# Performance work log

Hardware: AMD Instinct MI355X
Metric: run time of the kernel (lower is better)

Reference implementation:

```python
import jax, jax.numpy as jnp
import numpy as np

N = 118; DM = 768; DP = 128; DR = 128; DH = 256; DN = 256; DPHI = 192; DE = 256; NOUT = 2
T = 2048; NFEAT = 64
NEG = 0.01  # LeakyReLU default slope


def leaky(x):
    return jax.nn.leaky_relu(x, NEG)


def lstm(x, Wih, Whh, bih, bhh, last_only=False):
    # x: [B,T,F]; PyTorch gate order i,f,g,o
    B, Tt, _ = x.shape
    H = Whh.shape[1]
    xg = x @ Wih.T + (bih + bhh)  # [B,T,4H] precomputed input gates
    def step(carry, xt):
        h, c = carry
        g = xt + h @ Whh.T
        i, f, gg, o = jnp.split(g, 4, axis=-1)
        c = jax.nn.sigmoid(f) * c + jax.nn.sigmoid(i) * jnp.tanh(gg)
        h = jax.nn.sigmoid(o) * jnp.tanh(c)
        return (h, c), (None if last_only else h)
    init = (jnp.zeros((B, H), x.dtype), jnp.zeros((B, H), x.dtype))
    (h, c), hs = jax.lax.scan(step, init, jnp.swapaxes(xg, 0, 1))
    return h if last_only else jnp.swapaxes(hs, 0, 1)


def setup_inputs() -> dict:
    key = jax.random.key(0)
    ks = iter(jax.random.split(key, 40))
    def rn(shape, scale=0.05):
        return jax.random.normal(next(ks), shape, jnp.float32) * scale
    inp = {
        'x': jax.random.normal(next(ks), (N, T, NFEAT), jnp.float32),
        'x_message': jax.random.normal(next(ks), (N, DM), jnp.float32),
        'pseudo_message': rn((DM,), 1.0),
        'Wih0': rn((4 * DP, NFEAT)), 'Whh0': rn((4 * DP, DP)), 'bih0': rn((4 * DP,)), 'bhh0': rn((4 * DP,)),
        'Wih1': rn((4 * DP, DP)), 'Whh1': rn((4 * DP, DP)), 'bih1': rn((4 * DP,)), 'bhh1': rn((4 * DP,)),
        'Wum': rn((DM + 1, DR)), 'Wvm': rn((DM + 1, DR)),
        'Wup': rn((DP + 1, DR)), 'Wvp': rn((DP + 1, DR)),
        'Wpe': rn((2, 3 * DR)), 'bpe': rn((2,)),
        'Whyb': rn((DH, 3 * DR)), 'bhyb': rn((DH,)),
        'Wact': rn((DN, DH + 2)), 'bact': rn((DN,)),
        'Winact': rn((DN, DH)), 'binact': rn((DN,)),
        'Wphin': rn((2 * DN, DPHI)), 'aphi': rn((DPHI, 1)),
        'Won': rn((2 * DN, DN)), 'Weo': rn((3 * DN, DE)),
        'Wi': rn((N, DN + 2 * DE, NOUT)), 'bi': rn((N, NOUT)),
    }
    return inp


def reference(x, x_message, pseudo_message, Wih0, Whh0, bih0, bhh0, Wih1, Whh1, bih1, bhh1,
              Wum, Wvm, Wup, Wvp, Wpe, bpe, Whyb, bhyb, Wact, bact, Winact, binact,
              Wphin, aphi, Won, Weo, Wi, bi):
    h1 = lstm(x, Wih0, Whh0, bih0, bhh0)
    p = leaky(lstm(h1, Wih1, Whh1, bih1, bhh1, last_only=True))  # [N,DP]
    status = (jnp.sum(x_message, axis=-1) == 0).astype(x.dtype)  # [N]
    m = jnp.where(status[:, None] == 1, pseudo_message[None, :], x_message)
    st = status[:, None]  # [N,1]
    mc = jnp.concatenate([m, st], axis=1)
    pc = jnp.concatenate([p, st], axis=1)
    u_m = leaky(mc @ Wum); v_m = leaky(mc @ Wvm)
    u_p = leaky(pc @ Wup); v_p = leaky(pc @ Wvp)
    h_pmt = jax.nn.softmax(jnp.concatenate([u_m, u_m * v_p, v_p], 1) @ Wpe.T + bpe, axis=1)
    h_hyb = leaky(jnp.concatenate([u_p, u_p + v_m, v_m], 1) @ Whyb.T + bhyb)
    n_act = (jnp.concatenate([h_hyb, h_pmt], 1) @ Wact.T + bact) * (1 - st)
    n_in = (h_hyb @ Winact.T + binact) * st
    n = leaky(n_act + n_in)  # [N,DN]
    # pair[i,j] = concat(n[j], n[i]) matching torch repeat pattern
    pair = jnp.concatenate([jnp.broadcast_to(n[None, :, :], (N, N, DN)),
                            jnp.broadcast_to(n[:, None, :], (N, N, DN))], axis=-1)
    phi = (leaky(pair @ Wphin) @ aphi)[..., 0]  # [N,N]
    V1 = status == 0; V0 = status == 1
    def gsm(ph, mask):  # softmax over selected rows, per column
        logits = jnp.where(mask[:, None], ph, -1e30)
        return jnp.where(mask[:, None], jax.nn.softmax(logits, axis=0), ph)
    alpha = gsm(gsm(phi, V1), V0)
    e = jnp.concatenate([leaky(pair @ Won), pair], axis=-1) @ Weo  # [N,N,DE]
    hm1 = leaky(jnp.einsum('ij,ijd->id', (1 - st) * alpha, e))
    hm0 = leaky(jnp.einsum('ij,ijd->id', st * alpha, e))
    output = jnp.concatenate([n, hm0, hm1], axis=-1)  # [N, DN+2*DE]
    y_hat = jax.nn.softmax(jnp.einsum('nd,ndo->no', output, Wi) + bi, axis=1)
    l_ort = jnp.sqrt(jnp.sum((Wum @ Wvm.T) ** 2)) + jnp.sqrt(jnp.sum((Wup @ Wvp.T) ** 2))
    # vectorized pairwise cosine-sim * sign polarity over V1 nodes
    a = h_pmt[:, 1] - h_pmt[:, 0]
    w = jnp.where(V1, jnp.sign(a), 0.0)
    nn_ = n / jnp.maximum(jnp.linalg.norm(n, axis=1, keepdims=True), 1e-8)
    l_pol = jnp.sum((nn_ @ nn_.T) * (w[:, None] * w[None, :]))
    return y_hat, h_pmt, l_ort, l_pol
```

## Files before the change

kernel.cpp:

```cpp
#include <hip/hip_runtime.h>
#include <hip/hip_bf16.h>
#include <math.h>

#define NN 118
#define TT 2048
#define NF 64
#define DP 128
#define DN 256

typedef float v2f __attribute__((ext_vector_type(2)));

__device__ __forceinline__ float leaky(float x) { return x > 0.f ? x : 0.01f * x; }

__device__ __forceinline__ float waveRedSum(float v) {
#pragma unroll
    for (int off = 32; off > 0; off >>= 1) v += __shfl_down(v, off, 64);
    return v;
}
__device__ __forceinline__ float waveRedMax(float v) {
#pragma unroll
    for (int off = 32; off > 0; off >>= 1) v = fmaxf(v, __shfl_down(v, off, 64));
    return v;
}

__device__ __forceinline__ float sigmoidf_(float x) { return 1.0f / (1.0f + __expf(-x)); }
__device__ __forceinline__ float tanhf_(float x) { return 1.0f - 2.0f / (__expf(2.0f * x) + 1.0f); }

__device__ __forceinline__ float quad_sum(float v) {
    v += __int_as_float(__builtin_amdgcn_mov_dpp(__float_as_int(v), 0xB1, 0xF, 0xF, true));
    v += __int_as_float(__builtin_amdgcn_mov_dpp(__float_as_int(v), 0x4E, 0xF, 0xF, true));
    return v;
}

template <int KK>
__global__ __launch_bounds__(256) void xg_gemm(
    const float* __restrict__ A, const float* __restrict__ W,
    const float* __restrict__ b1, const float* __restrict__ b2,
    float* __restrict__ out, int rowStride, int rowOff, int lgTc) {
    int m0 = blockIdx.x * 64, n0 = blockIdx.y * 64;
    int tid = threadIdx.x, tx = tid & 15, ty = tid >> 4;
    __shared__ __align__(16) float As[64][KK + 4];
    __shared__ __align__(16) float Bs[64][KK + 4];
    const int SL = KK / 4;
    const int NL = 64 * SL / 256;
    int Tcm = (1 << lgTc) - 1;
#pragma unroll
    for (int r = 0; r < NL; r++) {
        int f = r * 256 + tid;
        int mm = f / SL, kv = f % SL;
        int m = m0 + mm;
        int grow = (m >> lgTc) * rowStride + (m & Tcm) + rowOff;
        *(float4*)&As[mm][4 * kv] = *(const float4*)&A[(size_t)grow * KK + 4 * kv];
        *(float4*)&Bs[mm][4 * kv] = *(const float4*)&W[(size_t)(n0 + mm) * KK + 4 * kv];
    }
    __syncthreads();
    float acc[4][4] = {};
#pragma unroll 4
    for (int kk = 0; kk < SL; kk++) {
        float4 a4[4], b4[4];
#pragma unroll
        for (int i = 0; i < 4; i++) a4[i] = *(const float4*)&As[4 * ty + i][4 * kk];
#pragma unroll
        for (int i = 0; i < 4; i++) b4[i] = *(const float4*)&Bs[tx + 16 * i][4 * kk];
#pragma unroll
        for (int i = 0; i < 4; i++)
#pragma unroll
            for (int jj = 0; jj < 4; jj++)
                acc[i][jj] += a4[i].x * b4[jj].x + a4[i].y * b4[jj].y +
                              a4[i].z * b4[jj].z + a4[i].w * b4[jj].w;
    }
#pragma unroll
    for (int jj = 0; jj < 4; jj++) {
        int col = n0 + tx + 16 * jj;
        float bb = b1[col] + b2[col];
#pragma unroll
        for (int i = 0; i < 4; i++) {
            size_t row = m0 + 4 * ty + i;
            out[row * 512 + col] = acc[i][jj] + bb;
        }
    }
}

#define LOADW(r, j) \
    float4 t##r##_##j = *(const float4*)&Whh[(size_t)(g + 128 * (r)) * 128 + kq * 32 + 4 * (j)]; \
    v2f w##r##_##j##a = {t##r##_##j.x, t##r##_##j.y}; \
    v2f w##r##_##j##b = {t##r##_##j.z, t##r##_##j.w};
#define LOADW_R(r) LOADW(r, 0) LOADW(r, 1) LOADW(r, 2) LOADW(r, 3) \
                   LOADW(r, 4) LOADW(r, 5) LOADW(r, 6) LOADW(r, 7)
#define DOTJ(j) { \
    float4 hv4 = h4[j]; \
    v2f hl = {hv4.x, hv4.y}; v2f hh = {hv4.z, hv4.w}; \
    acc0 += w0_##j##a * hl; acc0 += w0_##j##b * hh; \
    acc1 += w1_##j##a * hl; acc1 += w1_##j##b * hh; \
    acc2 += w2_##j##a * hl; acc2 += w2_##j##b * hh; \
    acc3 += w3_##j##a * hl; acc3 += w3_##j##b * hh; }

__global__ void
__attribute__((amdgpu_flat_work_group_size(512, 512), amdgpu_waves_per_eu(2, 2)))
lstm2_rec(
    const float* __restrict__ xg0, const float* __restrict__ xg1,
    const float* __restrict__ Whh0, const float* __restrict__ Whh1,
    float* __restrict__ h0s, float* __restrict__ c0s,
    float* __restrict__ h1s, float* __restrict__ c1s,
    float* __restrict__ h1c, float* __restrict__ p_out,
    int phase, int nch, int Tc) {
    int layer = blockIdx.y;
    if (layer == 0 && phase >= nch) return;
    if (layer == 1 && phase == 0) return;
    const float* __restrict__ xg  = layer ? xg1 : xg0;
    const float* __restrict__ Whh = layer ? Whh1 : Whh0;
    float* hs = layer ? h1s : h0s;
    float* cs = layer ? c1s : c0s;
    int t_start = (layer ? (phase - 1) : phase) * Tc;

    int b = blockIdx.x, t = threadIdx.x;
    int g = t >> 2, kq = t & 3;
    __shared__ __align__(16) float hb[2][160];

    LOADW_R(0) LOADW_R(1) LOADW_R(2) LOADW_R(3)

    float c = 0.f;
    float xc0 = 0.f, xc1 = 0.f, xc2 = 0.f, xc3 = 0.f;
    const float* xgb = xg + (size_t)b * Tc * 512;
    if (kq == 0) {
        c = cs[b * 128 + g];
        xc0 = xgb[g]; xc1 = xgb[g + 128]; xc2 = xgb[g + 256]; xc3 = xgb[g + 384];
    }
    if (t < 128) hb[0][(t >> 5) * 36 + (t & 31)] = hs[b * 128 + t];
    __syncthreads();

    int cur = 0;
    float h = 0.f;
#pragma unroll 1
    for (int tl = 0; tl < Tc; tl++) {
        float xn0 = 0.f, xn1 = 0.f, xn2 = 0.f, xn3 = 0.f;
        if (kq == 0 && tl + 1 < Tc) {
            const float* xr = &xgb[(size_t)(tl + 1) * 512];
            xn0 = xr[g]; xn1 = xr[g + 128]; xn2 = xr[g + 256]; xn3 = xr[g + 384];
        }
        v2f acc0 = {0.f, 0.f}, acc1 = {0.f, 0.f}, acc2 = {0.f, 0.f}, acc3 = {0.f, 0.f};
        const float4* h4 = (const float4*)&hb[cur][kq * 36];
        DOTJ(0) DOTJ(1) DOTJ(2) DOTJ(3) DOTJ(4) DOTJ(5) DOTJ(6) DOTJ(7)
        float a0 = quad_sum(acc0.x + acc0.y);
        float a1 = quad_sum(acc1.x + acc1.y);
        float a2 = quad_sum(acc2.x + acc2.y);
        float a3 = quad_sum(acc3.x + acc3.y);
        if (kq == 0) {
            float gi = a0 + xc0, gf = a1 + xc1, gg = a2 + xc2, go = a3 + xc3;
            c = sigmoidf_(gf) * c + sigmoidf_(gi) * tanhf_(gg);
            h = sigmoidf_(go) * tanhf_(c);
            hb[cur ^ 1][(g >> 5) * 36 + (g & 31)] = h;
            if (layer == 0) {
                h1c[(size_t)(b * Tc + tl) * 128 + g] = h;
            } else if (t_start + tl == TT - 1) {
                p_out[b * 128 + g] = leaky(h);
            }
            xc0 = xn0; xc1 = xn1; xc2 = xn2; xc3 = xn3;
        }
        __syncthreads();
        cur ^= 1;
    }
    if (kq == 0) { cs[b * 128 + g] = c; hs[b * 128 + g] = h; }
}

__global__ __launch_bounds__(256) void head1_kernel(
    const float* __restrict__ x_message, const float* __restrict__ pseudo,
    const float* __restrict__ p_out,
    const float* __restrict__ Wum, const float* __restrict__ Wvm,
    const float* __restrict__ Wup, const float* __restrict__ Wvp,
    const float* __restrict__ Wpe, const float* __restrict__ bpe,
    const float* __restrict__ Whyb, const float* __restrict__ bhyb,
    const float* __restrict__ Wact, const float* __restrict__ bact,
    const float* __restrict__ Winact, const float* __restrict__ binact,
    const float* __restrict__ Wphin, const float* __restrict__ Won,
    const float* __restrict__ Weo,
    float* __restrict__ st_out, float* __restrict__ n_out, float* __restrict__ wnn_out,
    float* __restrict__ R_out, float* __restrict__ S_out,
    float* __restrict__ P_out, float* __restrict__ Q_out,
    float* __restrict__ A_out, float* __restrict__ B_out,
    float* __restrict__ d_out) {
    int i = blockIdx.x, tid = threadIdx.x;
    __shared__ float mc[769];
    __shared__ float pcp[128];
    __shared__ float um[128], vm[128], up[128], vp[128];
    __shared__ float hyb[256], nsh[256];
    __shared__ float red[4];
    __shared__ float sred[2][2];
    __shared__ float st_sh, hp0_sh, hp1_sh, wpol_sh, norm_sh;

    float s = 0.f;
    for (int q = tid; q < 768; q += 256) s += x_message[i * 768 + q];
    s = waveRedSum(s);
    if ((tid & 63) == 0) red[tid >> 6] = s;
    __syncthreads();
    if (tid == 0) {
        float tot = red[0] + red[1] + red[2] + red[3];
        float st = (tot == 0.f) ? 1.f : 0.f;
        st_sh = st; st_out[i] = st;
    }
    __syncthreads();
    float st = st_sh;
    for (int q = tid; q < 768; q += 256)
        mc[q] = (st == 1.f) ? pseudo[q] : x_message[i * 768 + q];
    if (tid == 0) mc[768] = st;
    if (tid < 128) pcp[tid] = p_out[i * 128 + tid];
    __syncthreads();

    if (tid < 128) {
        int d = tid;
        float a0 = 0.f;
        for (int q = 0; q < 769; q++) a0 += mc[q] * Wum[q * 128 + d];
        um[d] = leaky(a0);
        float a1 = 0.f;
        for (int q = 0; q < 128; q++) a1 += pcp[q] * Wup[q * 128 + d];
        a1 += st * Wup[128 * 128 + d];
        up[d] = leaky(a1);
    } else {
        int d = tid - 128;
        float a0 = 0.f;
        for (int q = 0; q < 769; q++) a0 += mc[q] * Wvm[q * 128 + d];
        vm[d] = leaky(a0);
        float a1 = 0.f;
        for (int q = 0; q < 128; q++) a1 += pcp[q] * Wvp[q * 128 + d];
        a1 += st * Wvp[128 * 128 + d];
        vp[d] = leaky(a1);
    }
    __syncthreads();

    float t0 = 0.f, t1 = 0.f;
    if (tid < 128) {
        int d = tid;
        float um_d = um[d], vp_d = vp[d], uv = um_d * vp_d;
        t0 = um_d * Wpe[d] + uv * Wpe[128 + d] + vp_d * Wpe[256 + d];
        t1 = um_d * Wpe[384 + d] + uv * Wpe[384 + 128 + d] + vp_d * Wpe[384 + 256 + d];
    }
    t0 = waveRedSum(t0); t1 = waveRedSum(t1);
    if (tid < 128 && (tid & 63) == 0) { sred[0][tid >> 6] = t0; sred[1][tid >> 6] = t1; }
    __syncthreads();
    if (tid == 0) {
        float z0 = sred[0][0] + sred[0][1] + bpe[0];
        float z1 = sred[1][0] + sred[1][1] + bpe[1];
        float mx = fmaxf(z0, z1);
        float e0 = __expf(z0 - mx), e1 = __expf(z1 - mx);
        float inv = 1.f / (e0 + e1);
        float h0 = e0 * inv, h1 = e1 * inv;
        d_out[236 + i * 2 + 0] = h0; d_out[236 + i * 2 + 1] = h1;
        hp0_sh = h0; hp1_sh = h1;
        float sgn = (z1 > z0) ? 1.f : ((z1 < z0) ? -1.f : 0.f);
        wpol_sh = (st == 0.f) ? sgn : 0.f;
    }
    __syncthreads();

    {
        float acc = bhyb[tid];
        const float* Wr = Whyb + tid * 384;
        for (int q = 0; q < 128; q++) {
            float upq = up[q], vmq = vm[q];
            acc += upq * Wr[q] + (upq + vmq) * Wr[128 + q] + vmq * Wr[256 + q];
        }
        hyb[tid] = leaky(acc);
    }
    __syncthreads();

    {
        float hp0 = hp0_sh, hp1 = hp1_sh;
        float aa = bact[tid];
        float ai = binact[tid];
        const float* Wr = Wact + tid * 258;
        const float* Wr2 = Winact + tid * 256;
        for (int q = 0; q < 256; q++) { float h = hyb[q]; aa += h * Wr[q]; ai += h * Wr2[q]; }
        aa += hp0 * Wr[256] + hp1 * Wr[257];
        float nv = leaky(aa * (1.f - st) + ai * st);
        nsh[tid] = nv; n_out[i * 256 + tid] = nv;
    }
    __syncthreads();

    float nv = nsh[tid];
    float ssum = waveRedSum(nv * nv);
    if ((tid & 63) == 0) red[tid >> 6] = ssum;
    __syncthreads();
    if (tid == 0) norm_sh = fmaxf(sqrtf(red[0] + red[1] + red[2] + red[3]), 1e-8f);
    __syncthreads();
    wnn_out[i * 256 + tid] = wpol_sh * nv / norm_sh;

    if (tid < 192) {
        float r = 0.f, sc = 0.f;
        for (int q = 0; q < 256; q++) {
            float nq = nsh[q];
            r += nq * Wphin[q * 192 + tid];
            sc += nq * Wphin[(256 + q) * 192 + tid];
        }
        R_out[i * 192 + tid] = r; S_out[i * 192 + tid] = sc;
    }
    {
        float pa = 0.f, qa = 0.f, aa = 0.f, ba = 0.f;
        for (int q = 0; q < 256; q++) {
            float nq = nsh[q];
            pa += nq * Won[q * 256 + tid];
            qa += nq * Won[(256 + q) * 256 + tid];
            aa += nq * Weo[(256 + q) * 256 + tid];
            ba += nq * Weo[(512 + q) * 256 + tid];
        }
        P_out[i * 256 + tid] = pa; Q_out[i * 256 + tid] = qa;
        A_out[i * 256 + tid] = aa; B_out[i * 256 + tid] = ba;
    }
}

__global__ __launch_bounds__(128) void lort_kernel(
    const float* __restrict__ Wum, const float* __restrict__ Wvm,
    const float* __restrict__ Wup, const float* __restrict__ Wvp,
    float* __restrict__ lort) {
    int k = blockIdx.x, l = threadIdx.x, which = blockIdx.y;
    const float* Am = which ? Wup : Wum;
    const float* Bm = which ? Wvp : Wvm;
    int Rr = which ? 129 : 769;
    float g1 = 0.f, g2 = 0.f;
    for (int m = 0; m < Rr; m++) {
        g1 += Am[m * 128 + k] * Am[m * 128 + l];
        g2 += Bm[m * 128 + k] * Bm[m * 128 + l];
    }
    float p = waveRedSum(g1 * g2);
    if ((l & 63) == 0) atomicAdd(&lort[which], p);
}

__global__ __launch_bounds__(128) void phi_kernel(
    const float* __restrict__ R, const float* __restrict__ S,
    const float* __restrict__ aphi, float* __restrict__ phi_cm) {
    int j = blockIdx.x, tid = threadIdx.x;
    __shared__ float rj[192], ap[192];
    for (int q = tid; q < 192; q += 128) { rj[q] = R[j * 192 + q]; ap[q] = aphi[q]; }
    __syncthreads();
    if (tid < NN) {
        const float* Si = S + tid * 192;
        float acc = 0.f;
        for (int d = 0; d < 192; d++) acc += leaky(rj[d] + Si[d]) * ap[d];
        phi_cm[j * NN + tid] = acc;
    }
}

__global__ __launch_bounds__(128) void alpha_kernel(
    const float* __restrict__ phi_cm, const float* __restrict__ stv,
    float* __restrict__ w0_cm, float* __restrict__ w1_cm) {
    int j = blockIdx.x, tid = threadIdx.x;
    __shared__ float sm[2][2], ssum[2][2];
    bool act = tid < NN;
    float sti = act ? stv[tid] : -1.f;
    float v = act ? phi_cm[j * NN + tid] : 0.f;
    float m0 = (sti == 0.f) ? v : -3.0e38f;
    float m1 = (sti == 1.f) ? v : -3.0e38f;
    float M0 = waveRedMax(m0), M1 = waveRedMax(m1);
    if ((tid & 63) == 0) { sm[tid >> 6][0] = M0; sm[tid >> 6][1] = M1; }
    __syncthreads();
    M0 = fmaxf(sm[0][0], sm[1][0]); M1 = fmaxf(sm[0][1], sm[1][1]);
    float e = 0.f;
    if (act) e = __expf(v - ((sti == 0.f) ? M0 : M1));
    float e0 = (sti == 0.f) ? e : 0.f, e1 = (sti == 1.f) ? e : 0.f;
    float S0 = waveRedSum(e0), S1 = waveRedSum(e1);
    if ((tid & 63) == 0) { ssum[tid >> 6][0] = S0; ssum[tid >> 6][1] = S1; }
    __syncthreads();
    S0 = ssum[0][0] + ssum[1][0]; S1 = ssum[0][1] + ssum[1][1];
    if (act) {
        float alpha = e / ((sti == 0.f) ? S0 : S1);
        w0_cm[j * NN + tid] = sti * alpha;
        w1_cm[j * NN + tid] = (1.f - sti) * alpha;
    }
}

__global__ __launch_bounds__(256) void qsum_kernel(
    const float* __restrict__ P, const float* __restrict__ Q, const float* __restrict__ Ab,
    const float* __restrict__ w0_cm, const float* __restrict__ w1_cm,
    float* __restrict__ qs0, float* __restrict__ qs1,
    float* __restrict__ as0, float* __restrict__ as1,
    float* __restrict__ ws0, float* __restrict__ ws1) {
    int i = blockIdx.x, d = threadIdx.x;
    float Qd = Q[i * 256 + d];
    float q0 = 0.f, q1 = 0.f, a0 = 0.f, a1 = 0.f, s0 = 0.f, s1 = 0.f;
    for (int jj = 0; jj < NN; jj++) {
        float w0 = w0_cm[jj * NN + i], w1 = w1_cm[jj * NN + i];
        float pq = leaky(P[jj * 256 + d] + Qd);
        float av = Ab[jj * 256 + d];
        q0 += w0 * pq; q1 += w1 * pq;
        a0 += w0 * av; a1 += w1 * av;
        s0 += w0; s1 += w1;
    }
    qs0[i * 256 + d] = q0; qs1[i * 256 + d] = q1;
    as0[i * 256 + d] = a0; as1[i * 256 + d] = a1;
    if (d == 0) { ws0[i] = s0; ws1[i] = s1; }
}

__global__ __launch_bounds__(256) void hm_out_kernel(
    const float* __restrict__ qs0, const float* __restrict__ qs1,
    const float* __restrict__ as0, const float* __restrict__ as1,
    const float* __restrict__ ws0, const float* __restrict__ ws1,
    const float* __restrict__ Bb, const float* __restrict__ nbuf,
    const float* __restrict__ Weo, const float* __restrict__ Wi,
    const float* __restrict__ bi, float* __restrict__ d_out) {
    int i = blockIdx.x, d = threadIdx.x;
    __shared__ float q0sh[256], q1sh[256];
    __shared__ float r0[4], r1[4];
    q0sh[d] = qs0[i * 256 + d]; q1sh[d] = qs1[i * 256 + d];
    __syncthreads();
    float Bd = Bb[i * 256 + d];
    float h0 = as0[i * 256 + d] + ws0[i] * Bd;
    float h1 = as1[i * 256 + d] + ws1[i] * Bd;
    for (int k = 0; k < 256; k++) {
        float w = Weo[k * 256 + d];
        h0 += q0sh[k] * w; h1 += q1sh[k] * w;
    }
    h0 = leaky(h0); h1 = leaky(h1);
    float nd = nbuf[i * 256 + d];
    const float* Wii = Wi + (size_t)i * 1536;
    float l0 = nd * Wii[d * 2] + h0 * Wii[(256 + d) * 2] + h1 * Wii[(512 + d) * 2];
    float l1 = nd * Wii[d * 2 + 1] + h0 * Wii[(256 + d) * 2 + 1] + h1 * Wii[(512 + d) * 2 + 1];
    l0 = waveRedSum(l0); l1 = waveRedSum(l1);
    if ((d & 63) == 0) { r0[d >> 6] = l0; r1[d >> 6] = l1; }
    __syncthreads();
    if (d == 0) {
        float z0 = r0[0] + r0[1] + r0[2] + r0[3] + bi[i * 2 + 0];
        float z1 = r1[0] + r1[1] + r1[2] + r1[3] + bi[i * 2 + 1];
        float mx = fmaxf(z0, z1);
        float e0 = __expf(z0 - mx), e1 = __expf(z1 - mx);
        float inv = 1.f / (e0 + e1);
        d_out[i * 2 + 0] = e0 * inv;
        d_out[i * 2 + 1] = e1 * inv;
    }
}

__global__ __launch_bounds__(256) void pol_kernel(
    const float* __restrict__ wnn, const float* __restrict__ lort,
    float* __restrict__ d_out) {
    int d = threadIdx.x;
    __shared__ float red[4];
    float s = 0.f;
    for (int i = 0; i < NN; i++) s += wnn[i * 256 + d];
    float p = waveRedSum(s * s);
    if ((d & 63) == 0) red[d >> 6] = p;
    __syncthreads();
    if (d == 0) {
        d_out[473] = red[0] + red[1] + red[2] + red[3];
        d_out[472] = sqrtf(lort[0]) + sqrtf(lort[1]);
    }
}

extern "C" void kernel_launch(void* const* d_in, const int* in_sizes, int n_in,
                              void* d_out_v, int out_size, void* d_ws, size_t ws_size,
                              hipStream_t stream) {
    (void)in_sizes; (void)n_in; (void)out_size;
    const float* x        = (const float*)d_in[0];
    const float* x_msg    = (const float*)d_in[1];
    const float* pseudo   = (const float*)d_in[2];
    const float* Wih0     = (const float*)d_in[3];
    const float* Whh0     = (const float*)d_in[4];
    const float* bih0     = (const float*)d_in[5];
    const float* bhh0     = (const float*)d_in[6];
    const float* Wih1     = (const float*)d_in[7];
    const float* Whh1     = (const float*)d_in[8];
    const float* bih1     = (const float*)d_in[9];
    const float* bhh1     = (const float*)d_in[10];
    const float* Wum      = (const float*)d_in[11];
    const float* Wvm      = (const float*)d_in[12];
    const float* Wup      = (const float*)d_in[13];
    const float* Wvp      = (const float*)d_in[14];
    const float* Wpe      = (const float*)d_in[15];
    const float* bpe      = (const float*)d_in[16];
    const float* Whyb     = (const float*)d_in[17];
    const float* bhyb     = (const float*)d_in[18];
    const float* Wact     = (const float*)d_in[19];
    const float* bact     = (const float*)d_in[20];
    const float* Winact   = (const float*)d_in[21];
    const float* binact   = (const float*)d_in[22];
    const float* Wphin    = (const float*)d_in[23];
    const float* aphi     = (const float*)d_in[24];
    const float* Won      = (const float*)d_in[25];
    const float* Weo      = (const float*)d_in[26];
    const float* Wi       = (const float*)d_in[27];
    const float* bi       = (const float*)d_in[28];
    float* out = (float*)d_out_v;

    char* wsb = (char*)d_ws;
    size_t off = 0;
    auto alloc = [&](size_t nfloats) {
        float* p = (float*)(wsb + off);
        off += ((nfloats * 4 + 255) / 256) * 256;
        return p;
    };
    float* h0s   = alloc(NN * 128);
    float* c0s   = alloc(NN * 128);
    float* h1s   = alloc(NN * 128);
    float* c1s   = alloc(NN * 128);
    float* lort  = alloc(2);
    float* stb   = alloc(NN);
    float* p_out = alloc(NN * 128);
    float* nbuf  = alloc(NN * 256);
    float* wnn   = alloc(NN * 256);
    float* Rb    = alloc(NN * 192);
    float* Sb    = alloc(NN * 192);
    float* Pb    = alloc(NN * 256);
    float* Qb    = alloc(NN * 256);
    float* Ab    = alloc(NN * 256);
    float* Bb    = alloc(NN * 256);
    float* qs0   = alloc(NN * 256);
    float* qs1   = alloc(NN * 256);
    float* as0   = alloc(NN * 256);
    float* as1   = alloc(NN * 256);
    float* ws0   = alloc(NN);
    float* ws1   = alloc(NN);
    float* phicm = alloc(NN * NN);
    float* w0cm  = alloc(NN * NN);
    float* w1cm  = alloc(NN * NN);

    size_t remain = (ws_size > off) ? (ws_size - off) : 0;
    int Tc = 2048;
    while (Tc > 64 && (size_t)NN * Tc * (512 + 512 + 128) * 4 > remain) Tc >>= 1;
    float* xg0 = alloc((size_t)NN * Tc * 512);
    float* xg1 = alloc((size_t)NN * Tc * 512);
    float* h1c = alloc((size_t)NN * Tc * 128);
    int lgTc = __builtin_ctz(Tc);

    hipMemsetAsync(h0s, 0, (size_t)4 * NN * 128 * sizeof(float), stream);
    hipMemsetAsync(lort, 0, 2 * sizeof(float), stream);

    int nch = TT / Tc;
    dim3 gg((NN * Tc) / 64, 8);
    xg_gemm<64><<<gg, 256, 0, stream>>>(x, Wih0, bih0, bhh0, xg0, TT, 0, lgTc);
    for (int p = 0; p <= nch; p++) {
        lstm2_rec<<<dim3(NN, 2), 512, 0, stream>>>(xg0, xg1, Whh0, Whh1,
                                                   h0s, c0s, h1s, c1s,
                                                   h1c, p_out, p, nch, Tc);
        if (p < nch)
            xg_gemm<128><<<gg, 256, 0, stream>>>(h1c, Wih1, bih1, bhh1, xg1, Tc, 0, lgTc);
        if (p + 1 < nch)
            xg_gemm<64><<<gg, 256, 0, stream>>>(x, Wih0, bih0, bhh0, xg0, TT, (p + 1) * Tc, lgTc);
    }
    head1_kernel<<<NN, 256, 0, stream>>>(x_msg, pseudo, p_out, Wum, Wvm, Wup, Wvp,
                                         Wpe, bpe, Whyb, bhyb, Wact, bact, Winact, binact,
                                         Wphin, Won, Weo,
                                         stb, nbuf, wnn, Rb, Sb, Pb, Qb, Ab, Bb, out);
    lort_kernel<<<dim3(128, 2), 128, 0, stream>>>(Wum, Wvm, Wup, Wvp, lort);
    phi_kernel<<<NN, 128, 0, stream>>>(Rb, Sb, aphi, phicm);
    alpha_kernel<<<NN, 128, 0, stream>>>(phicm, stb, w0cm, w1cm);
    qsum_kernel<<<NN, 256, 0, stream>>>(Pb, Qb, Ab, w0cm, w1cm, qs0, qs1, as0, as1, ws0, ws1);
    hm_out_kernel<<<NN, 256, 0, stream>>>(qs0, qs1, as0, as1, ws0, ws1, Bb, nbuf, Weo, Wi, bi, out);
    pol_kernel<<<1, 256, 0, stream>>>(wnn, lort, out);
}
```

Measured before the change: 3.870 ms.

## Split LSTM recurrence across 8 lanes per gate with LDS-staged weights

```diff
diff --git a/kernel.cpp b/kernel.cpp
--- a/kernel.cpp
+++ b/kernel.cpp
@@ -26,9 +26,10 @@
 __device__ __forceinline__ float sigmoidf_(float x) { return 1.0f / (1.0f + __expf(-x)); }
 __device__ __forceinline__ float tanhf_(float x) { return 1.0f - 2.0f / (__expf(2.0f * x) + 1.0f); }
 
-__device__ __forceinline__ float quad_sum(float v) {
+__device__ __forceinline__ float red8(float v) {
     v += __int_as_float(__builtin_amdgcn_mov_dpp(__float_as_int(v), 0xB1, 0xF, 0xF, true));
     v += __int_as_float(__builtin_amdgcn_mov_dpp(__float_as_int(v), 0x4E, 0xF, 0xF, true));
+    v += __int_as_float(__builtin_amdgcn_ds_swizzle(__float_as_int(v), 0x101F));
     return v;
 }
 
@@ -81,12 +82,22 @@
     }
 }
 
+#define STAGE(c) { \
+    __syncthreads(); \
+    _Pragma("unroll") \
+    for (int k = 0; k < 4; k++) { \
+        int f = t + 1024 * k; \
+        float4 v = *(const float4*)&Whh[(size_t)(c) * 16384 + 4 * f]; \
+        *(float4*)&wst[(f >> 5) * 132 + (f & 31) * 4] = v; \
+    } \
+    __syncthreads(); }
+
 #define LOADW(r, j) \
-    float4 t##r##_##j = *(const float4*)&Whh[(size_t)(g + 128 * (r)) * 128 + kq * 32 + 4 * (j)]; \
+    float4 t##r##_##j = *(const float4*)&wst[g * 132 + kq * 16 + 4 * (j)]; \
     v2f w##r##_##j##a = {t##r##_##j.x, t##r##_##j.y}; \
     v2f w##r##_##j##b = {t##r##_##j.z, t##r##_##j.w};
-#define LOADW_R(r) LOADW(r, 0) LOADW(r, 1) LOADW(r, 2) LOADW(r, 3) \
-                   LOADW(r, 4) LOADW(r, 5) LOADW(r, 6) LOADW(r, 7)
+#define LOADW_R(r) LOADW(r, 0) LOADW(r, 1) LOADW(r, 2) LOADW(r, 3)
+
 #define DOTJ(j) { \
     float4 hv4 = h4[j]; \
     v2f hl = {hv4.x, hv4.y}; v2f hh = {hv4.z, hv4.w}; \
@@ -96,7 +107,7 @@
     acc3 += w3_##j##a * hl; acc3 += w3_##j##b * hh; }
 
 __global__ void
-__attribute__((amdgpu_flat_work_group_size(512, 512), amdgpu_waves_per_eu(2, 2)))
+__attribute__((amdgpu_flat_work_group_size(1024, 1024), amdgpu_waves_per_eu(4, 4)))
 lstm2_rec(
     const float* __restrict__ xg0, const float* __restrict__ xg1,
     const float* __restrict__ Whh0, const float* __restrict__ Whh1,
@@ -114,19 +125,19 @@
     int t_start = (layer ? (phase - 1) : phase) * Tc;
 
     int b = blockIdx.x, t = threadIdx.x;
-    int g = t >> 2, kq = t & 3;
-    __shared__ __align__(16) float hb[2][160];
-
-    LOADW_R(0) LOADW_R(1) LOADW_R(2) LOADW_R(3)
-
-    float c = 0.f;
-    float xc0 = 0.f, xc1 = 0.f, xc2 = 0.f, xc3 = 0.f;
+    int g = t >> 3, kq = t & 7;
+    __shared__ __align__(16) float wst[128 * 132];
+
+    STAGE(0) LOADW_R(0)
+    STAGE(1) LOADW_R(1)
+    STAGE(2) LOADW_R(2)
+    STAGE(3) LOADW_R(3)
+    __syncthreads();
+
+    float c = cs[b * 128 + g];
     const float* xgb = xg + (size_t)b * Tc * 512;
-    if (kq == 0) {
-        c = cs[b * 128 + g];
-        xc0 = xgb[g]; xc1 = xgb[g + 128]; xc2 = xgb[g + 256]; xc3 = xgb[g + 384];
-    }
-    if (t < 128) hb[0][(t >> 5) * 36 + (t & 31)] = hs[b * 128 + t];
+    float xc0 = xgb[g], xc1 = xgb[g + 128], xc2 = xgb[g + 256], xc3 = xgb[g + 384];
+    if (t < 128) wst[(t >> 4) * 20 + (t & 15)] = hs[b * 128 + t];
     __syncthreads();
 
     int cur = 0;
@@ -134,29 +145,29 @@
 #pragma unroll 1
     for (int tl = 0; tl < Tc; tl++) {
         float xn0 = 0.f, xn1 = 0.f, xn2 = 0.f, xn3 = 0.f;
-        if (kq == 0 && tl + 1 < Tc) {
+        if (tl + 1 < Tc) {
             const float* xr = &xgb[(size_t)(tl + 1) * 512];
             xn0 = xr[g]; xn1 = xr[g + 128]; xn2 = xr[g + 256]; xn3 = xr[g + 384];
         }
         v2f acc0 = {0.f, 0.f}, acc1 = {0.f, 0.f}, acc2 = {0.f, 0.f}, acc3 = {0.f, 0.f};
-        const float4* h4 = (const float4*)&hb[cur][kq * 36];
-        DOTJ(0) DOTJ(1) DOTJ(2) DOTJ(3) DOTJ(4) DOTJ(5) DOTJ(6) DOTJ(7)
-        float a0 = quad_sum(acc0.x + acc0.y);
-        float a1 = quad_sum(acc1.x + acc1.y);
-        float a2 = quad_sum(acc2.x + acc2.y);
-        float a3 = quad_sum(acc3.x + acc3.y);
+        const float4* h4 = (const float4*)&wst[cur * 160 + kq * 20];
+        DOTJ(0) DOTJ(1) DOTJ(2) DOTJ(3)
+        float a0 = red8(acc0.x + acc0.y);
+        float a1 = red8(acc1.x + acc1.y);
+        float a2 = red8(acc2.x + acc2.y);
+        float a3 = red8(acc3.x + acc3.y);
+        float gi = a0 + xc0, gf = a1 + xc1, gg = a2 + xc2, go = a3 + xc3;
+        c = sigmoidf_(gf) * c + sigmoidf_(gi) * tanhf_(gg);
+        h = sigmoidf_(go) * tanhf_(c);
         if (kq == 0) {
-            float gi = a0 + xc0, gf = a1 + xc1, gg = a2 + xc2, go = a3 + xc3;
-            c = sigmoidf_(gf) * c + sigmoidf_(gi) * tanhf_(gg);
-            h = sigmoidf_(go) * tanhf_(c);
-            hb[cur ^ 1][(g >> 5) * 36 + (g & 31)] = h;
+            wst[(cur ^ 1) * 160 + (g >> 4) * 20 + (g & 15)] = h;
             if (layer == 0) {
                 h1c[(size_t)(b * Tc + tl) * 128 + g] = h;
             } else if (t_start + tl == TT - 1) {
                 p_out[b * 128 + g] = leaky(h);
             }
-            xc0 = xn0; xc1 = xn1; xc2 = xn2; xc3 = xn3;
         }
+        xc0 = xn0; xc1 = xn1; xc2 = xn2; xc3 = xn3;
         __syncthreads();
         cur ^= 1;
     }
@@ -524,9 +535,9 @@
     dim3 gg((NN * Tc) / 64, 8);
     xg_gemm<64><<<gg, 256, 0, stream>>>(x, Wih0, bih0, bhh0, xg0, TT, 0, lgTc);
     for (int p = 0; p <= nch; p++) {
-        lstm2_rec<<<dim3(NN, 2), 512, 0, stream>>>(xg0, xg1, Whh0, Whh1,
-                                                   h0s, c0s, h1s, c1s,
-                                                   h1c, p_out, p, nch, Tc);
+        lstm2_rec<<<dim3(NN, 2), 1024, 0, stream>>>(xg0, xg1, Whh0, Whh1,
+                                                    h0s, c0s, h1s, c1s,
+                                                    h1c, p_out, p, nch, Tc);
         if (p < nch)
             xg_gemm<128><<<gg, 256, 0, stream>>>(h1c, Wih1, bih1, bhh1, xg1, Tc, 0, lgTc);
         if (p + 1 < nch)
```

Measured after the change: 4.142 ms. +7.0%, slower.
